# Performance work log

Measured on AMD Instinct MI355X. Metric: run time of the kernel, lower is better.

## Reference

```python
import jax, jax.numpy as jnp
import numpy as np

B, T, I, H = 32, 2048, 512, 512


def setup_inputs() -> dict:
    key = jax.random.key(0)
    ks = jax.random.split(key, 5)
    s_ih = 1.0 / np.sqrt(H)
    return {
        "x_t": jax.random.normal(ks[0], (B, T, I), dtype=jnp.float32),
        # PyTorch LSTM params, gate order [i, f, g, o]
        "W_ih": jax.random.uniform(ks[1], (4 * H, I), minval=-s_ih, maxval=s_ih, dtype=jnp.float32),
        "W_hh": jax.random.uniform(ks[2], (4 * H, H), minval=-s_ih, maxval=s_ih, dtype=jnp.float32),
        "b_ih": jax.random.uniform(ks[3], (4 * H,), minval=-s_ih, maxval=s_ih, dtype=jnp.float32),
        "b_hh": jax.random.uniform(ks[4], (4 * H,), minval=-s_ih, maxval=s_ih, dtype=jnp.float32),
    }


def _lstm_last_h(x_t, W_ih, W_hh, b_ih, b_hh):
    Bx = x_t.shape[0]
    Hh = W_hh.shape[1]
    # Precompute input projections for all timesteps in one big GEMM: [B,T,4H]
    x_proj = jnp.einsum("bti,gi->btg", x_t, W_ih) + (b_ih + b_hh)

    def step(carry, xp_t):
        h, c = carry
        z = xp_t + h @ W_hh.T  # [B, 4H]
        i, f, g, o = jnp.split(z, 4, axis=-1)
        i = jax.nn.sigmoid(i)
        f = jax.nn.sigmoid(f)
        g = jnp.tanh(g)
        o = jax.nn.sigmoid(o)
        c = f * c + i * g
        h = o * jnp.tanh(c)
        return (h, c), None

    h0 = jnp.zeros((Bx, Hh), dtype=x_t.dtype)
    c0 = jnp.zeros((Bx, Hh), dtype=x_t.dtype)
    (h_T, _), _ = jax.lax.scan(step, (h0, c0), jnp.swapaxes(x_proj, 0, 1))
    return h_T[None, :, :]  # [1, B, H] to match torch (num_layers*dirs, B, H)


def reference(x_t, W_ih, W_hh, b_ih, b_hh):
    return _lstm_last_h(x_t, W_ih, W_hh, b_ih, b_hh)
```

## Files before the change

kernel.cpp:

```cpp
#include <hip/hip_runtime.h>


#define T_FULL 2048
#define CHUNK  256
#define NCHUNK 8
#define NBLK   32

typedef float  f32x4 __attribute__((ext_vector_type(4)));
typedef short  s16x8 __attribute__((ext_vector_type(8)));

#define MFMA16(a,b,c) __builtin_amdgcn_mfma_f32_16x16x32_bf16((a),(b),(c),0,0,0)

__device__ inline unsigned short f2bf(float f){
  unsigned u = __builtin_bit_cast(unsigned, f);
  u += 0x7fffu + ((u>>16)&1u);
  return (unsigned short)(u>>16);
}
__device__ inline float bf2f(unsigned short s){
  unsigned u = ((unsigned)s)<<16;
  return __builtin_bit_cast(float, u);
}
__device__ inline float sigmoid_(float x){
  x = fminf(fmaxf(x,-30.f),30.f);
  return 1.f/(1.f + __expf(-x));
}
__device__ inline float tanh_(float x){
  x = fminf(fmaxf(x,-15.f),15.f);
  float e = __expf(2.f*x);
  return (e-1.f)/(e+1.f);
}

__global__ __launch_bounds__(256) void lstm_p1(
    const float* __restrict__ x, const float* __restrict__ Wih,
    const float* __restrict__ bih, const float* __restrict__ bhh,
    unsigned short* __restrict__ xp, int t0)
{
  __shared__ __align__(16) unsigned short At[64*136];
  __shared__ __align__(16) unsigned short Bt[64*136];
  const int tid = threadIdx.x, lane = tid&63, w = tid>>6;
  const int l15 = lane&15, l4 = lane>>4;
  const int n0 = blockIdx.x*64, m0 = blockIdx.y*64;
  const int mbase = (w&1)*32, nbase = (w>>1)*32;

  f32x4 acc[2][2];
  #pragma unroll
  for (int mi=0; mi<2; ++mi)
    #pragma unroll
    for (int ni=0; ni<2; ++ni)
      acc[mi][ni] = (f32x4){0.f,0.f,0.f,0.f};

  for (int kb=0; kb<4; ++kb){
    #pragma unroll
    for (int it=0; it<4; ++it){
      int grp = it*256 + tid;
      int row = grp>>4, c8 = (grp&15)*8;
      {
        int m = m0 + row;
        size_t t = (size_t)t0 + (m>>5), b = (size_t)(m&31);
        const float* src = x + ((b*2048 + t)<<9) + kb*128 + c8;
        f32x4 v0 = *(const f32x4*)src, v1 = *(const f32x4*)(src+4);
        unsigned short* d = &At[row*136 + c8];
        d[0]=f2bf(v0[0]); d[1]=f2bf(v0[1]); d[2]=f2bf(v0[2]); d[3]=f2bf(v0[3]);
        d[4]=f2bf(v1[0]); d[5]=f2bf(v1[1]); d[6]=f2bf(v1[2]); d[7]=f2bf(v1[3]);
      }
      {
        const float* src = Wih + (size_t)(n0+row)*512 + kb*128 + c8;
        f32x4 v0 = *(const f32x4*)src, v1 = *(const f32x4*)(src+4);
        unsigned short* d = &Bt[row*136 + c8];
        d[0]=f2bf(v0[0]); d[1]=f2bf(v0[1]); d[2]=f2bf(v0[2]); d[3]=f2bf(v0[3]);
        d[4]=f2bf(v1[0]); d[5]=f2bf(v1[1]); d[6]=f2bf(v1[2]); d[7]=f2bf(v1[3]);
      }
    }
    __syncthreads();
    #pragma unroll
    for (int ks=0; ks<4; ++ks){
      s16x8 af0 = *(const s16x8*)&At[(mbase+   l15)*136 + ks*32 + l4*8];
      s16x8 af1 = *(const s16x8*)&At[(mbase+16+l15)*136 + ks*32 + l4*8];
      s16x8 bf0 = *(const s16x8*)&Bt[(nbase+   l15)*136 + ks*32 + l4*8];
      s16x8 bf1 = *(const s16x8*)&Bt[(nbase+16+l15)*136 + ks*32 + l4*8];
      acc[0][0] = MFMA16(af0,bf0,acc[0][0]);
      acc[0][1] = MFMA16(af0,bf1,acc[0][1]);
      acc[1][0] = MFMA16(af1,bf0,acc[1][0]);
      acc[1][1] = MFMA16(af1,bf1,acc[1][1]);
    }
    __syncthreads();
  }
  #pragma unroll
  for (int ni=0; ni<2; ++ni){
    int col = n0 + nbase + ni*16 + l15;
    float bias = bih[col] + bhh[col];
    #pragma unroll
    for (int mi=0; mi<2; ++mi){
      #pragma unroll
      for (int r=0; r<4; ++r){
        int mrow = m0 + mbase + mi*16 + l4*4 + r;
        xp[(size_t)mrow*2048 + col] = f2bf(acc[mi][ni][r] + bias);
      }
    }
  }
}

__global__ __launch_bounds__(256) void lstm_p2(
    const unsigned short* __restrict__ xp, const float* __restrict__ Whh,
    unsigned short* __restrict__ Hbuf, float* __restrict__ cst,
    unsigned int* __restrict__ flag, float* __restrict__ out, int t0)
{
  const int k = blockIdx.x;
  const int tid = threadIdx.x;
  const int lane = tid & 63, w = tid >> 6;
  const int l15 = lane & 15, l4 = lane >> 4;
  const int mt = w & 1, gp = w >> 1;

  __shared__ __align__(16) char Hl[32*1024];
  __shared__ float zl[32][68];

  s16x8 wf[2][16];
  #pragma unroll
  for (int nt=0; nt<2; ++nt){
    int lrow = gp*32 + nt*16 + l15;
    int grow = (lrow>>4)*512 + k*16 + (lrow&15);
    const float* wr = Whh + (size_t)grow*512;
    #pragma unroll
    for (int ks=0; ks<16; ++ks){
      const float* s = wr + ks*32 + l4*8;
      f32x4 v0 = *(const f32x4*)s, v1 = *(const f32x4*)(s+4);
      s16x8 tt;
      tt[0]=(short)f2bf(v0[0]); tt[1]=(short)f2bf(v0[1]);
      tt[2]=(short)f2bf(v0[2]); tt[3]=(short)f2bf(v0[3]);
      tt[4]=(short)f2bf(v1[0]); tt[5]=(short)f2bf(v1[1]);
      tt[6]=(short)f2bf(v1[2]); tt[7]=(short)f2bf(v1[3]);
      wf[nt][ks] = tt;
    }
  }

  const int s_ = tid >> 3, a_ = tid & 7;
  const int ucol = k*16 + 2*a_;
  float c0 = cst[s_*512 + ucol], c1 = cst[s_*512 + ucol + 1];

  for (int tt=0; tt<CHUNK; ++tt){
    const int t = t0 + tt;

    unsigned int xq[4];
    #pragma unroll
    for (int g=0; g<4; ++g)
      xq[g] = *(const unsigned int*)(xp + (size_t)(tt*32 + s_)*2048 + g*512 + ucol);

    if (t > 0){
      if (w == 0){
        unsigned v;
        do {
          v = (lane < NBLK)
            ? __hip_atomic_load(&flag[lane<<5], __ATOMIC_RELAXED, __HIP_MEMORY_SCOPE_AGENT)
            : 0xffffffffu;
        } while (!__all(v >= (unsigned)t));
        __builtin_amdgcn_fence(__ATOMIC_ACQUIRE, "agent");
      }
      __syncthreads();
    }

    {
      const char* hsrc = (const char*)(Hbuf + ((t+1)&1)*(32*512));
      #pragma unroll
      for (int it=0; it<8; ++it){
        int off = (it*256 + tid)*16;
        f32x4 v = *(const f32x4*)(hsrc + off);
        *(f32x4*)&Hl[off ^ (((off>>10)&7)<<4)] = v;
      }
    }
    __syncthreads();

    f32x4 acc0 = (f32x4){0.f,0.f,0.f,0.f};
    f32x4 acc1 = (f32x4){0.f,0.f,0.f,0.f};
    {
      const int row = mt*16 + l15;
      const int swz = (row&7)<<4;
      const int rbase = row<<10;
      #pragma unroll
      for (int ks=0; ks<16; ++ks){
        int cb = ks*64 + l4*16;
        s16x8 af = *(const s16x8*)&Hl[rbase | (cb ^ swz)];
        acc0 = MFMA16(af, wf[0][ks], acc0);
        acc1 = MFMA16(af, wf[1][ks], acc1);
      }
    }
    #pragma unroll
    for (int r=0; r<4; ++r){
      zl[mt*16 + l4*4 + r][gp*32 +      l15] = acc0[r];
      zl[mt*16 + l4*4 + r][gp*32 + 16 + l15] = acc1[r];
    }
    __syncthreads();

    float zi0 = zl[s_][ 0 + 2*a_    ] + bf2f((unsigned short)(xq[0]&0xffffu));
    float zi1 = zl[s_][ 0 + 2*a_ + 1] + bf2f((unsigned short)(xq[0]>>16));
    float zf0 = zl[s_][16 + 2*a_    ] + bf2f((unsigned short)(xq[1]&0xffffu));
    float zf1 = zl[s_][16 + 2*a_ + 1] + bf2f((unsigned short)(xq[1]>>16));
    float zg0 = zl[s_][32 + 2*a_    ] + bf2f((unsigned short)(xq[2]&0xffffu));
    float zg1 = zl[s_][32 + 2*a_ + 1] + bf2f((unsigned short)(xq[2]>>16));
    float zo0 = zl[s_][48 + 2*a_    ] + bf2f((unsigned short)(xq[3]&0xffffu));
    float zo1 = zl[s_][48 + 2*a_ + 1] + bf2f((unsigned short)(xq[3]>>16));

    float i0 = sigmoid_(zi0), f0 = sigmoid_(zf0), g0 = tanh_(zg0), o0 = sigmoid_(zo0);
    float i1 = sigmoid_(zi1), f1 = sigmoid_(zf1), g1 = tanh_(zg1), o1 = sigmoid_(zo1);
    c0 = f0*c0 + i0*g0;
    c1 = f1*c1 + i1*g1;
    float h0 = o0 * tanh_(c0);
    float h1 = o1 * tanh_(c1);

    {
      unsigned short* hdst = Hbuf + (t&1)*(32*512);
      unsigned int hp = (unsigned int)f2bf(h0) | ((unsigned int)f2bf(h1)<<16);
      __hip_atomic_store((unsigned int*)((char*)hdst + s_*1024 + ucol*2), hp,
                         __ATOMIC_RELAXED, __HIP_MEMORY_SCOPE_AGENT);
    }
    if (t == T_FULL-1){
      out[s_*512 + ucol    ] = h0;
      out[s_*512 + ucol + 1] = h1;
    }

    asm volatile("s_waitcnt vmcnt(0)" ::: "memory");
    __syncthreads();
    if (tid == 0)
      __hip_atomic_store(&flag[k<<5], (unsigned)(t+1),
                         __ATOMIC_RELAXED, __HIP_MEMORY_SCOPE_AGENT);
  }

  cst[s_*512 + ucol    ] = c0;
  cst[s_*512 + ucol + 1] = c1;
}

extern "C" void kernel_launch(void* const* d_in, const int* in_sizes, int n_in,
                              void* d_out, int out_size, void* d_ws, size_t ws_size,
                              hipStream_t stream)
{
  const float* x   = (const float*)d_in[0];
  const float* Wih = (const float*)d_in[1];
  const float* Whh = (const float*)d_in[2];
  const float* bih = (const float*)d_in[3];
  const float* bhh = (const float*)d_in[4];
  float* out = (float*)d_out;

  char* ws = (char*)d_ws;
  const size_t XP_BYTES = (size_t)CHUNK*32*2048*2;
  unsigned short* xp   = (unsigned short*)ws;
  unsigned short* Hbuf = (unsigned short*)(ws + XP_BYTES);
  float*          cst  = (float*)(ws + XP_BYTES + 65536);
  unsigned int*   flag = (unsigned int*)(ws + XP_BYTES + 131072);

  (void)hipMemsetAsync(Hbuf, 0, 65536 + 65536 + 4096, stream);

  for (int c=0; c<NCHUNK; ++c){
    int t0 = c*CHUNK;
    lstm_p1<<<dim3(32, CHUNK*32/64), 256, 0, stream>>>(x, Wih, bih, bhh, xp, t0);
    lstm_p2<<<NBLK, 256, 0, stream>>>(xp, Whh, Hbuf, cst, flag, out, t0);
  }
}
```

Before: 6.382 ms.

## Replace per-step flag barrier with tagged hidden-state words polled directly

Each hidden-state element is now stored as a 32-bit word holding the bf16 value in its high half and the timestep tag in its low half, in a 4-deep ring buffer. Consumers poll the values directly from global memory until every tag matches, removing the separate flag array, the block-wide syncthreads and the staging of h in LDS. The gate layout is also remapped so that each wave owns whole units, with the four gates exchanged by lane shuffles rather than through shared memory. The cost is twice the global traffic for h, spinning on a full row load, and correctness that depends on the tagged words becoming visible atomically.

```diff
diff --git a/kernel.cpp b/kernel.cpp
--- a/kernel.cpp
+++ b/kernel.cpp
@@ -8,6 +8,8 @@
 
 typedef float  f32x4 __attribute__((ext_vector_type(4)));
 typedef short  s16x8 __attribute__((ext_vector_type(8)));
+typedef unsigned int u32;
+typedef u32    u32x4 __attribute__((ext_vector_type(4)));
 
 #define MFMA16(a,b,c) __builtin_amdgcn_mfma_f32_16x16x32_bf16((a),(b),(c),0,0,0)
 
@@ -100,26 +102,26 @@
   }
 }
 
-__global__ __launch_bounds__(256) void lstm_p2(
+__global__ __launch_bounds__(256,1) void lstm_p2(
     const unsigned short* __restrict__ xp, const float* __restrict__ Whh,
-    unsigned short* __restrict__ Hbuf, float* __restrict__ cst,
-    unsigned int* __restrict__ flag, float* __restrict__ out, int t0)
+    u32* __restrict__ H32, float* __restrict__ cst,
+    float* __restrict__ out, int t0)
 {
   const int k = blockIdx.x;
   const int tid = threadIdx.x;
   const int lane = tid & 63, w = tid >> 6;
   const int l15 = lane & 15, l4 = lane >> 4;
-  const int mt = w & 1, gp = w >> 1;
-
-  __shared__ __align__(16) char Hl[32*1024];
-  __shared__ float zl[32][68];
-
-  s16x8 wf[2][16];
-  #pragma unroll
-  for (int nt=0; nt<2; ++nt){
-    int lrow = gp*32 + nt*16 + l15;
-    int grow = (lrow>>4)*512 + k*16 + (lrow&15);
-    const float* wr = Whh + (size_t)grow*512;
+  const int u_local = l15 >> 2, g = l15 & 3;
+  const int U = k*16 + w*4 + u_local;
+  const int gcol = g*512 + U;
+
+  const int q = g;
+  const int mt_q = q >> 1, rr = (q & 1) * 2;
+  const int bq = mt_q*16 + l4*4 + rr;
+
+  s16x8 wf[16];
+  {
+    const float* wr = Whh + (size_t)(g*512 + U)*512;
     #pragma unroll
     for (int ks=0; ks<16; ++ks){
       const float* s = wr + ks*32 + l4*8;
@@ -129,103 +131,117 @@
       tt[2]=(short)f2bf(v0[2]); tt[3]=(short)f2bf(v0[3]);
       tt[4]=(short)f2bf(v1[0]); tt[5]=(short)f2bf(v1[1]);
       tt[6]=(short)f2bf(v1[2]); tt[7]=(short)f2bf(v1[3]);
-      wf[nt][ks] = tt;
-    }
-  }
-
-  const int s_ = tid >> 3, a_ = tid & 7;
-  const int ucol = k*16 + 2*a_;
-  float c0 = cst[s_*512 + ucol], c1 = cst[s_*512 + ucol + 1];
+      wf[ks] = tt;
+    }
+  }
+
+  float c[2][4];
+  #pragma unroll
+  for (int mt2=0; mt2<2; ++mt2)
+    #pragma unroll
+    for (int r=0; r<4; ++r)
+      c[mt2][r] = cst[(size_t)(mt2*16 + l4*4 + r)*512 + U];
 
   for (int tt=0; tt<CHUNK; ++tt){
     const int t = t0 + tt;
-
-    unsigned int xq[4];
-    #pragma unroll
-    for (int g=0; g<4; ++g)
-      xq[g] = *(const unsigned int*)(xp + (size_t)(tt*32 + s_)*2048 + g*512 + ucol);
-
-    if (t > 0){
-      if (w == 0){
-        unsigned v;
-        do {
-          v = (lane < NBLK)
-            ? __hip_atomic_load(&flag[lane<<5], __ATOMIC_RELAXED, __HIP_MEMORY_SCOPE_AGENT)
-            : 0xffffffffu;
-        } while (!__all(v >= (unsigned)t));
+    const u32 tagc = (u32)t, tagn = (u32)(t+1);
+    const u32* Hs = H32 + (size_t)(t & 3)*16384;
+    u32*       Hd = H32 + (size_t)((t+1) & 3)*16384;
+
+    float xg[2][4];
+    #pragma unroll
+    for (int mt2=0; mt2<2; ++mt2)
+      #pragma unroll
+      for (int r=0; r<4; ++r)
+        xg[mt2][r] = bf2f(xp[(size_t)(tt*32 + mt2*16 + l4*4 + r)*2048 + gcol]);
+
+    f32x4 z[2];
+    #pragma unroll
+    for (int mt2=0; mt2<2; ++mt2){
+      u32x4 A0[16], A1[16];
+      u32 bad;
+      do {
         __builtin_amdgcn_fence(__ATOMIC_ACQUIRE, "agent");
-      }
-      __syncthreads();
+        const u32* rowp = Hs + (mt2*16 + l15)*512 + l4*8;
+        #pragma unroll
+        for (int ks=0; ks<16; ++ks){
+          A0[ks] = *(const u32x4*)(rowp + ks*32);
+          A1[ks] = *(const u32x4*)(rowp + ks*32 + 4);
+        }
+        bad = 0;
+        #pragma unroll
+        for (int ks=0; ks<16; ++ks){
+          #pragma unroll
+          for (int j=0; j<4; ++j){
+            bad |= (A0[ks][j] ^ tagc);
+            bad |= (A1[ks][j] ^ tagc);
+          }
+        }
+        bad &= 0xffffu;
+      } while (__any(bad != 0));
+
+      f32x4 acc = (f32x4){0.f,0.f,0.f,0.f};
+      #pragma unroll
+      for (int ks=0; ks<16; ++ks){
+        u32x4 p;
+        p[0] = (A0[ks][0] >> 16) | (A0[ks][1] & 0xffff0000u);
+        p[1] = (A0[ks][2] >> 16) | (A0[ks][3] & 0xffff0000u);
+        p[2] = (A1[ks][0] >> 16) | (A1[ks][1] & 0xffff0000u);
+        p[3] = (A1[ks][2] >> 16) | (A1[ks][3] & 0xffff0000u);
+        s16x8 af = __builtin_bit_cast(s16x8, p);
+        acc = MFMA16(af, wf[ks], acc);
+      }
+      z[mt2] = acc;
+    }
+
+    float hv[2][4];
+    #pragma unroll
+    for (int mt2=0; mt2<2; ++mt2){
+      #pragma unroll
+      for (int r=0; r<4; ++r){
+        float v = z[mt2][r] + xg[mt2][r];
+        float vi = __shfl_xor(v, g    );
+        float vf = __shfl_xor(v, g ^ 1);
+        float vg = __shfl_xor(v, g ^ 2);
+        float vo = __shfl_xor(v, g ^ 3);
+        float ii = sigmoid_(vi), ff = sigmoid_(vf);
+        float gg = tanh_(vg),    oo = sigmoid_(vo);
+        float cc = ff*c[mt2][r] + ii*gg;
+        c[mt2][r] = cc;
+        hv[mt2][r] = oo * tanh_(cc);
+      }
     }
 
     {
-      const char* hsrc = (const char*)(Hbuf + ((t+1)&1)*(32*512));
-      #pragma unroll
-      for (int it=0; it<8; ++it){
-        int off = (it*256 + tid)*16;
-        f32x4 v = *(const f32x4*)(hsrc + off);
-        *(f32x4*)&Hl[off ^ (((off>>10)&7)<<4)] = v;
-      }
-    }
-    __syncthreads();
-
-    f32x4 acc0 = (f32x4){0.f,0.f,0.f,0.f};
-    f32x4 acc1 = (f32x4){0.f,0.f,0.f,0.f};
-    {
-      const int row = mt*16 + l15;
-      const int swz = (row&7)<<4;
-      const int rbase = row<<10;
-      #pragma unroll
-      for (int ks=0; ks<16; ++ks){
-        int cb = ks*64 + l4*16;
-        s16x8 af = *(const s16x8*)&Hl[rbase | (cb ^ swz)];
-        acc0 = MFMA16(af, wf[0][ks], acc0);
-        acc1 = MFMA16(af, wf[1][ks], acc1);
-      }
-    }
-    #pragma unroll
-    for (int r=0; r<4; ++r){
-      zl[mt*16 + l4*4 + r][gp*32 +      l15] = acc0[r];
-      zl[mt*16 + l4*4 + r][gp*32 + 16 + l15] = acc1[r];
-    }
-    __syncthreads();
-
-    float zi0 = zl[s_][ 0 + 2*a_    ] + bf2f((unsigned short)(xq[0]&0xffffu));
-    float zi1 = zl[s_][ 0 + 2*a_ + 1] + bf2f((unsigned short)(xq[0]>>16));
-    float zf0 = zl[s_][16 + 2*a_    ] + bf2f((unsigned short)(xq[1]&0xffffu));
-    float zf1 = zl[s_][16 + 2*a_ + 1] + bf2f((unsigned short)(xq[1]>>16));
-    float zg0 = zl[s_][32 + 2*a_    ] + bf2f((unsigned short)(xq[2]&0xffffu));
-    float zg1 = zl[s_][32 + 2*a_ + 1] + bf2f((unsigned short)(xq[2]>>16));
-    float zo0 = zl[s_][48 + 2*a_    ] + bf2f((unsigned short)(xq[3]&0xffffu));
-    float zo1 = zl[s_][48 + 2*a_ + 1] + bf2f((unsigned short)(xq[3]>>16));
-
-    float i0 = sigmoid_(zi0), f0 = sigmoid_(zf0), g0 = tanh_(zg0), o0 = sigmoid_(zo0);
-    float i1 = sigmoid_(zi1), f1 = sigmoid_(zf1), g1 = tanh_(zg1), o1 = sigmoid_(zo1);
-    c0 = f0*c0 + i0*g0;
-    c1 = f1*c1 + i1*g1;
-    float h0 = o0 * tanh_(c0);
-    float h1 = o1 * tanh_(c1);
-
-    {
-      unsigned short* hdst = Hbuf + (t&1)*(32*512);
-      unsigned int hp = (unsigned int)f2bf(h0) | ((unsigned int)f2bf(h1)<<16);
-      __hip_atomic_store((unsigned int*)((char*)hdst + s_*1024 + ucol*2), hp,
+      float ha0 = (q&1) ? hv[0][2] : hv[0][0];
+      float ha1 = (q&1) ? hv[0][3] : hv[0][1];
+      float hb0 = (q&1) ? hv[1][2] : hv[1][0];
+      float hb1 = (q&1) ? hv[1][3] : hv[1][1];
+      float h0 = (q>>1) ? hb0 : ha0;
+      float h1 = (q>>1) ? hb1 : ha1;
+      u32 w0 = ((u32)f2bf(h0) << 16) | tagn;
+      u32 w1 = ((u32)f2bf(h1) << 16) | tagn;
+      __hip_atomic_store(&Hd[(size_t)(bq  )*512 + U], w0,
                          __ATOMIC_RELAXED, __HIP_MEMORY_SCOPE_AGENT);
-    }
-    if (t == T_FULL-1){
-      out[s_*512 + ucol    ] = h0;
-      out[s_*512 + ucol + 1] = h1;
-    }
-
-    asm volatile("s_waitcnt vmcnt(0)" ::: "memory");
-    __syncthreads();
-    if (tid == 0)
-      __hip_atomic_store(&flag[k<<5], (unsigned)(t+1),
+      __hip_atomic_store(&Hd[(size_t)(bq+1)*512 + U], w1,
                          __ATOMIC_RELAXED, __HIP_MEMORY_SCOPE_AGENT);
-  }
-
-  cst[s_*512 + ucol    ] = c0;
-  cst[s_*512 + ucol + 1] = c1;
+      if (t == T_FULL-1){
+        out[(size_t)(bq  )*512 + U] = h0;
+        out[(size_t)(bq+1)*512 + U] = h1;
+      }
+    }
+  }
+
+  {
+    float ca0 = (q&1) ? c[0][2] : c[0][0];
+    float ca1 = (q&1) ? c[0][3] : c[0][1];
+    float cb0 = (q&1) ? c[1][2] : c[1][0];
+    float cb1 = (q&1) ? c[1][3] : c[1][1];
+    float c0s = (q>>1) ? cb0 : ca0;
+    float c1s = (q>>1) ? cb1 : ca1;
+    cst[(size_t)(bq  )*512 + U] = c0s;
+    cst[(size_t)(bq+1)*512 + U] = c1s;
+  }
 }
 
 extern "C" void kernel_launch(void* const* d_in, const int* in_sizes, int n_in,
@@ -241,16 +257,15 @@
 
   char* ws = (char*)d_ws;
   const size_t XP_BYTES = (size_t)CHUNK*32*2048*2;
-  unsigned short* xp   = (unsigned short*)ws;
-  unsigned short* Hbuf = (unsigned short*)(ws + XP_BYTES);
-  float*          cst  = (float*)(ws + XP_BYTES + 65536);
-  unsigned int*   flag = (unsigned int*)(ws + XP_BYTES + 131072);
-
-  (void)hipMemsetAsync(Hbuf, 0, 65536 + 65536 + 4096, stream);
+  unsigned short* xp  = (unsigned short*)ws;
+  u32*            H32 = (u32*)(ws + XP_BYTES);
+  float*          cst = (float*)(ws + XP_BYTES + 262144);
+
+  (void)hipMemsetAsync(H32, 0, 262144 + 65536, stream);
 
   for (int c=0; c<NCHUNK; ++c){
     int t0 = c*CHUNK;
     lstm_p1<<<dim3(32, CHUNK*32/64), 256, 0, stream>>>(x, Wih, bih, bhh, xp, t0);
-    lstm_p2<<<NBLK, 256, 0, stream>>>(xp, Whh, Hbuf, cst, flag, out, t0);
-  }
-}
+    lstm_p2<<<NBLK, 256, 0, stream>>>(xp, Whh, H32, cst, out, t0);
+  }
+}
```

After: 24.98 ms. 3.91x slower.

## Split recurrent step into 128 single-wave blocks with per-batch-half sync groups

Applied to the files above, without the earlier changes.

The recurrent kernel changes from 32 four-wave blocks to 128 single-wave blocks, split into two independent batch halves of 64 blocks that each sync only among themselves through a 4-deep H ring buffer. Each wave loads its h fragments directly from global memory into registers instead of staging through LDS. Gate nonlinearities are combined via lane shuffles, which removes the LDS z-exchange and all __syncthreads from the step. The aim is to cut per-step latency on the serial critical path. In exchange it adds more spinning blocks polling flags and more global h reads per block.

```diff
diff --git a/kernel.cpp b/kernel.cpp
--- a/kernel.cpp
+++ b/kernel.cpp
@@ -4,10 +4,10 @@
 #define T_FULL 2048
 #define CHUNK  256
 #define NCHUNK 8
-#define NBLK   32
 
 typedef float  f32x4 __attribute__((ext_vector_type(4)));
 typedef short  s16x8 __attribute__((ext_vector_type(8)));
+typedef unsigned int u32;
 
 #define MFMA16(a,b,c) __builtin_amdgcn_mfma_f32_16x16x32_bf16((a),(b),(c),0,0,0)
 
@@ -100,132 +100,135 @@
   }
 }
 
-__global__ __launch_bounds__(256) void lstm_p2(
+__global__ __launch_bounds__(64,1) void lstm_p2(
     const unsigned short* __restrict__ xp, const float* __restrict__ Whh,
     unsigned short* __restrict__ Hbuf, float* __restrict__ cst,
-    unsigned int* __restrict__ flag, float* __restrict__ out, int t0)
+    u32* __restrict__ flag, float* __restrict__ out, int t0)
 {
-  const int k = blockIdx.x;
-  const int tid = threadIdx.x;
-  const int lane = tid & 63, w = tid >> 6;
+  const int lane = threadIdx.x;
+  const int c = blockIdx.x >> 6, s = blockIdx.x & 63;
   const int l15 = lane & 15, l4 = lane >> 4;
-  const int mt = w & 1, gp = w >> 1;
-
-  __shared__ __align__(16) char Hl[32*1024];
-  __shared__ float zl[32][68];
-
-  s16x8 wf[2][16];
+  const int g = l15 & 3, uq = l15 >> 2;
+  const int u0 = s*8 + uq, u1 = u0 + 4;
+
+  s16x8 wf0[16], wf1[16];
+  {
+    const float* w0 = Whh + (size_t)(g*512 + u0)*512 + l4*8;
+    const float* w1 = Whh + (size_t)(g*512 + u1)*512 + l4*8;
+    #pragma unroll
+    for (int ks=0; ks<16; ++ks){
+      f32x4 a0 = *(const f32x4*)(w0 + ks*32), b0 = *(const f32x4*)(w0 + ks*32 + 4);
+      f32x4 a1 = *(const f32x4*)(w1 + ks*32), b1 = *(const f32x4*)(w1 + ks*32 + 4);
+      s16x8 t0v, t1v;
+      t0v[0]=(short)f2bf(a0[0]); t0v[1]=(short)f2bf(a0[1]);
+      t0v[2]=(short)f2bf(a0[2]); t0v[3]=(short)f2bf(a0[3]);
+      t0v[4]=(short)f2bf(b0[0]); t0v[5]=(short)f2bf(b0[1]);
+      t0v[6]=(short)f2bf(b0[2]); t0v[7]=(short)f2bf(b0[3]);
+      t1v[0]=(short)f2bf(a1[0]); t1v[1]=(short)f2bf(a1[1]);
+      t1v[2]=(short)f2bf(a1[2]); t1v[3]=(short)f2bf(a1[3]);
+      t1v[4]=(short)f2bf(b1[0]); t1v[5]=(short)f2bf(b1[1]);
+      t1v[6]=(short)f2bf(b1[2]); t1v[7]=(short)f2bf(b1[3]);
+      wf0[ks] = t0v; wf1[ks] = t1v;
+    }
+  }
+
+  float c0[4], c1[4];
   #pragma unroll
-  for (int nt=0; nt<2; ++nt){
-    int lrow = gp*32 + nt*16 + l15;
-    int grow = (lrow>>4)*512 + k*16 + (lrow&15);
-    const float* wr = Whh + (size_t)grow*512;
-    #pragma unroll
-    for (int ks=0; ks<16; ++ks){
-      const float* s = wr + ks*32 + l4*8;
-      f32x4 v0 = *(const f32x4*)s, v1 = *(const f32x4*)(s+4);
-      s16x8 tt;
-      tt[0]=(short)f2bf(v0[0]); tt[1]=(short)f2bf(v0[1]);
-      tt[2]=(short)f2bf(v0[2]); tt[3]=(short)f2bf(v0[3]);
-      tt[4]=(short)f2bf(v1[0]); tt[5]=(short)f2bf(v1[1]);
-      tt[6]=(short)f2bf(v1[2]); tt[7]=(short)f2bf(v1[3]);
-      wf[nt][ks] = tt;
-    }
-  }
-
-  const int s_ = tid >> 3, a_ = tid & 7;
-  const int ucol = k*16 + 2*a_;
-  float c0 = cst[s_*512 + ucol], c1 = cst[s_*512 + ucol + 1];
+  for (int r=0; r<4; ++r){
+    c0[r] = cst[(size_t)(c*16 + l4*4 + r)*512 + u0];
+    c1[r] = cst[(size_t)(c*16 + l4*4 + r)*512 + u1];
+  }
 
   for (int tt=0; tt<CHUNK; ++tt){
     const int t = t0 + tt;
 
-    unsigned int xq[4];
-    #pragma unroll
-    for (int g=0; g<4; ++g)
-      xq[g] = *(const unsigned int*)(xp + (size_t)(tt*32 + s_)*2048 + g*512 + ucol);
-
-    if (t > 0){
-      if (w == 0){
-        unsigned v;
-        do {
-          v = (lane < NBLK)
-            ? __hip_atomic_load(&flag[lane<<5], __ATOMIC_RELAXED, __HIP_MEMORY_SCOPE_AGENT)
-            : 0xffffffffu;
-        } while (!__all(v >= (unsigned)t));
-        __builtin_amdgcn_fence(__ATOMIC_ACQUIRE, "agent");
-      }
-      __syncthreads();
-    }
-
-    {
-      const char* hsrc = (const char*)(Hbuf + ((t+1)&1)*(32*512));
+    float xg0[4], xg1[4];
+    {
+      const unsigned short* xrow = xp + (size_t)(tt*32 + c*16)*2048 + g*512;
       #pragma unroll
-      for (int it=0; it<8; ++it){
-        int off = (it*256 + tid)*16;
-        f32x4 v = *(const f32x4*)(hsrc + off);
-        *(f32x4*)&Hl[off ^ (((off>>10)&7)<<4)] = v;
-      }
-    }
-    __syncthreads();
+      for (int r=0; r<4; ++r){
+        xg0[r] = bf2f(xrow[(size_t)(l4*4+r)*2048 + u0]);
+        xg1[r] = bf2f(xrow[(size_t)(l4*4+r)*2048 + u1]);
+      }
+    }
+
+    {
+      u32 v;
+      do {
+        v = (lane == s) ? (u32)t
+          : __hip_atomic_load(&flag[(u32)((c<<6) | lane) << 4],
+                              __ATOMIC_RELAXED, __HIP_MEMORY_SCOPE_AGENT);
+      } while (__any(v < (u32)t));
+    }
+    __builtin_amdgcn_fence(__ATOMIC_ACQUIRE, "agent");
+
+    s16x8 hf[16];
+    {
+      const unsigned short* Hs = Hbuf + (size_t)((c<<2) | (t&3))*8192 + l15*512 + l4*8;
+      #pragma unroll
+      for (int ks=0; ks<16; ++ks)
+        hf[ks] = *(const s16x8*)(Hs + ks*32);
+    }
 
     f32x4 acc0 = (f32x4){0.f,0.f,0.f,0.f};
     f32x4 acc1 = (f32x4){0.f,0.f,0.f,0.f};
-    {
-      const int row = mt*16 + l15;
-      const int swz = (row&7)<<4;
-      const int rbase = row<<10;
-      #pragma unroll
-      for (int ks=0; ks<16; ++ks){
-        int cb = ks*64 + l4*16;
-        s16x8 af = *(const s16x8*)&Hl[rbase | (cb ^ swz)];
-        acc0 = MFMA16(af, wf[0][ks], acc0);
-        acc1 = MFMA16(af, wf[1][ks], acc1);
-      }
-    }
+    #pragma unroll
+    for (int ks=0; ks<16; ++ks){
+      acc0 = MFMA16(hf[ks], wf0[ks], acc0);
+      acc1 = MFMA16(hf[ks], wf1[ks], acc1);
+    }
+
+    float hv0[4], hv1[4];
     #pragma unroll
     for (int r=0; r<4; ++r){
-      zl[mt*16 + l4*4 + r][gp*32 +      l15] = acc0[r];
-      zl[mt*16 + l4*4 + r][gp*32 + 16 + l15] = acc1[r];
-    }
-    __syncthreads();
-
-    float zi0 = zl[s_][ 0 + 2*a_    ] + bf2f((unsigned short)(xq[0]&0xffffu));
-    float zi1 = zl[s_][ 0 + 2*a_ + 1] + bf2f((unsigned short)(xq[0]>>16));
-    float zf0 = zl[s_][16 + 2*a_    ] + bf2f((unsigned short)(xq[1]&0xffffu));
-    float zf1 = zl[s_][16 + 2*a_ + 1] + bf2f((unsigned short)(xq[1]>>16));
-    float zg0 = zl[s_][32 + 2*a_    ] + bf2f((unsigned short)(xq[2]&0xffffu));
-    float zg1 = zl[s_][32 + 2*a_ + 1] + bf2f((unsigned short)(xq[2]>>16));
-    float zo0 = zl[s_][48 + 2*a_    ] + bf2f((unsigned short)(xq[3]&0xffffu));
-    float zo1 = zl[s_][48 + 2*a_ + 1] + bf2f((unsigned short)(xq[3]>>16));
-
-    float i0 = sigmoid_(zi0), f0 = sigmoid_(zf0), g0 = tanh_(zg0), o0 = sigmoid_(zo0);
-    float i1 = sigmoid_(zi1), f1 = sigmoid_(zf1), g1 = tanh_(zg1), o1 = sigmoid_(zo1);
-    c0 = f0*c0 + i0*g0;
-    c1 = f1*c1 + i1*g1;
-    float h0 = o0 * tanh_(c0);
-    float h1 = o1 * tanh_(c1);
-
-    {
-      unsigned short* hdst = Hbuf + (t&1)*(32*512);
-      unsigned int hp = (unsigned int)f2bf(h0) | ((unsigned int)f2bf(h1)<<16);
-      __hip_atomic_store((unsigned int*)((char*)hdst + s_*1024 + ucol*2), hp,
+      float v = acc0[r] + xg0[r];
+      float vi = __shfl_xor(v, g    );
+      float vf = __shfl_xor(v, g ^ 1);
+      float vg = __shfl_xor(v, g ^ 2);
+      float vo = __shfl_xor(v, g ^ 3);
+      float ii = sigmoid_(vi), ff = sigmoid_(vf), gg = tanh_(vg), oo = sigmoid_(vo);
+      float cc = ff*c0[r] + ii*gg; c0[r] = cc; hv0[r] = oo*tanh_(cc);
+      v = acc1[r] + xg1[r];
+      vi = __shfl_xor(v, g    );
+      vf = __shfl_xor(v, g ^ 1);
+      vg = __shfl_xor(v, g ^ 2);
+      vo = __shfl_xor(v, g ^ 3);
+      ii = sigmoid_(vi); ff = sigmoid_(vf); gg = tanh_(vg); oo = sigmoid_(vo);
+      cc = ff*c1[r] + ii*gg; c1[r] = cc; hv1[r] = oo*tanh_(cc);
+    }
+
+    float hsel0 = (g&1) ? ((g&2) ? hv0[3] : hv0[1]) : ((g&2) ? hv0[2] : hv0[0]);
+    float hsel1 = (g&1) ? ((g&2) ? hv1[3] : hv1[1]) : ((g&2) ? hv1[2] : hv1[0]);
+
+    {
+      unsigned short* Hd = Hbuf + (size_t)((c<<2) | ((t+1)&3))*8192;
+      u32 hb0 = f2bf(hsel0), hb1 = f2bf(hsel1);
+      u32 o0 = (u32)__shfl_xor((int)hb0, 4);
+      u32 o1 = (u32)__shfl_xor((int)hb1, 4);
+      if ((uq & 1) == 0){
+        __hip_atomic_store((u32*)(Hd + (l4*4+g)*512 + u0), hb0 | (o0<<16),
+                           __ATOMIC_RELAXED, __HIP_MEMORY_SCOPE_AGENT);
+        __hip_atomic_store((u32*)(Hd + (l4*4+g)*512 + u1), hb1 | (o1<<16),
+                           __ATOMIC_RELAXED, __HIP_MEMORY_SCOPE_AGENT);
+      }
+      if (t == T_FULL-1){
+        out[(size_t)(c*16 + l4*4 + g)*512 + u0] = hsel0;
+        out[(size_t)(c*16 + l4*4 + g)*512 + u1] = hsel1;
+      }
+    }
+
+    asm volatile("s_waitcnt vmcnt(0)" ::: "memory");
+    if (lane == 0)
+      __hip_atomic_store(&flag[(u32)((c<<6) | s) << 4], (u32)(t+1),
                          __ATOMIC_RELAXED, __HIP_MEMORY_SCOPE_AGENT);
-    }
-    if (t == T_FULL-1){
-      out[s_*512 + ucol    ] = h0;
-      out[s_*512 + ucol + 1] = h1;
-    }
-
-    asm volatile("s_waitcnt vmcnt(0)" ::: "memory");
-    __syncthreads();
-    if (tid == 0)
-      __hip_atomic_store(&flag[k<<5], (unsigned)(t+1),
-                         __ATOMIC_RELAXED, __HIP_MEMORY_SCOPE_AGENT);
-  }
-
-  cst[s_*512 + ucol    ] = c0;
-  cst[s_*512 + ucol + 1] = c1;
+  }
+
+  {
+    float cs0 = (g&1) ? ((g&2) ? c0[3] : c0[1]) : ((g&2) ? c0[2] : c0[0]);
+    float cs1 = (g&1) ? ((g&2) ? c1[3] : c1[1]) : ((g&2) ? c1[2] : c1[0]);
+    cst[(size_t)(c*16 + l4*4 + g)*512 + u0] = cs0;
+    cst[(size_t)(c*16 + l4*4 + g)*512 + u1] = cs1;
+  }
 }
 
 extern "C" void kernel_launch(void* const* d_in, const int* in_sizes, int n_in,
@@ -243,14 +246,14 @@
   const size_t XP_BYTES = (size_t)CHUNK*32*2048*2;
   unsigned short* xp   = (unsigned short*)ws;
   unsigned short* Hbuf = (unsigned short*)(ws + XP_BYTES);
-  float*          cst  = (float*)(ws + XP_BYTES + 65536);
-  unsigned int*   flag = (unsigned int*)(ws + XP_BYTES + 131072);
-
-  (void)hipMemsetAsync(Hbuf, 0, 65536 + 65536 + 4096, stream);
+  float*          cst  = (float*)(ws + XP_BYTES + 131072);
+  u32*            flag = (u32*)(ws + XP_BYTES + 131072 + 65536);
+
+  (void)hipMemsetAsync(Hbuf, 0, 131072 + 65536 + 8192, stream);
 
   for (int c=0; c<NCHUNK; ++c){
     int t0 = c*CHUNK;
     lstm_p1<<<dim3(32, CHUNK*32/64), 256, 0, stream>>>(x, Wih, bih, bhh, xp, t0);
-    lstm_p2<<<NBLK, 256, 0, stream>>>(xp, Whh, Hbuf, cst, flag, out, t0);
-  }
-}
+    lstm_p2<<<128, 64, 0, stream>>>(xp, Whh, Hbuf, cst, flag, out, t0);
+  }
+}
```

After: 12.94 ms. 2.03x slower.

## Overlap next-chunk input projection GEMM with recurrent LSTM steps in one fused launch

Applied to the files above, without the earlier changes.

Fuses the input-projection GEMM and the recurrent kernel into one launch. Blocks 0–31 run the recurrence on the current chunk, while the other 224 blocks compute the next chunk's projection into a double buffer. The chunk size is halved so more chunks can pipeline, and the flag spin loop is unrolled to keep two loads in flight. The recurrence blocks must share CUs with the GEMM blocks, which adds bandwidth contention and could slow the latency-bound serial steps.

```diff
diff --git a/kernel.cpp b/kernel.cpp
--- a/kernel.cpp
+++ b/kernel.cpp
@@ -2,12 +2,14 @@
 
 
 #define T_FULL 2048
-#define CHUNK  256
-#define NCHUNK 8
+#define CHUNK  128
+#define NCHUNK 16
 #define NBLK   32
+#define NGEMM  224
 
 typedef float  f32x4 __attribute__((ext_vector_type(4)));
 typedef short  s16x8 __attribute__((ext_vector_type(8)));
+typedef unsigned int u32;
 
 #define MFMA16(a,b,c) __builtin_amdgcn_mfma_f32_16x16x32_bf16((a),(b),(c),0,0,0)
 
@@ -30,16 +32,16 @@
   return (e-1.f)/(e+1.f);
 }
 
-__global__ __launch_bounds__(256) void lstm_p1(
-    const float* __restrict__ x, const float* __restrict__ Wih,
-    const float* __restrict__ bih, const float* __restrict__ bhh,
-    unsigned short* __restrict__ xp, int t0)
-{
-  __shared__ __align__(16) unsigned short At[64*136];
-  __shared__ __align__(16) unsigned short Bt[64*136];
+__device__ void gemm_tile(const float* __restrict__ x, const float* __restrict__ Wih,
+                          const float* __restrict__ bih, const float* __restrict__ bhh,
+                          unsigned short* __restrict__ xp, int t0, int nx, int ny,
+                          char* smem)
+{
+  unsigned short* At = (unsigned short*)smem;
+  unsigned short* Bt = (unsigned short*)(smem + 17408);
   const int tid = threadIdx.x, lane = tid&63, w = tid>>6;
   const int l15 = lane&15, l4 = lane>>4;
-  const int n0 = blockIdx.x*64, m0 = blockIdx.y*64;
+  const int n0 = nx*64, m0 = ny*64;
   const int mbase = (w&1)*32, nbase = (w>>1)*32;
 
   f32x4 acc[2][2];
@@ -100,19 +102,42 @@
   }
 }
 
-__global__ __launch_bounds__(256) void lstm_p2(
-    const unsigned short* __restrict__ xp, const float* __restrict__ Whh,
+__global__ __launch_bounds__(256) void lstm_p1(
+    const float* __restrict__ x, const float* __restrict__ Wih,
+    const float* __restrict__ bih, const float* __restrict__ bhh,
+    unsigned short* __restrict__ xp, int t0)
+{
+  __shared__ __align__(16) char smem[34816];
+  gemm_tile(x, Wih, bih, bhh, xp, t0, blockIdx.x, blockIdx.y, smem);
+}
+
+__global__ __launch_bounds__(256,1) void lstm_fused(
+    const unsigned short* __restrict__ xp_cur,
+    const float* __restrict__ x, const float* __restrict__ Wih,
+    const float* __restrict__ bih, const float* __restrict__ bhh,
+    unsigned short* __restrict__ xp_next, const float* __restrict__ Whh,
     unsigned short* __restrict__ Hbuf, float* __restrict__ cst,
-    unsigned int* __restrict__ flag, float* __restrict__ out, int t0)
-{
-  const int k = blockIdx.x;
+    u32* __restrict__ flag, float* __restrict__ out, int t0, int do_gemm)
+{
+  __shared__ __align__(16) char smem[41472];
+  const int bid = blockIdx.x;
+
+  if (bid >= NBLK){
+    if (do_gemm){
+      const int t0n = t0 + CHUNK;
+      for (int tile = bid - NBLK; tile < 32*(CHUNK*32/64); tile += NGEMM)
+        gemm_tile(x, Wih, bih, bhh, xp_next, t0n, tile & 31, tile >> 5, smem);
+    }
+    return;
+  }
+
+  char* Hl = smem;
+  float (*zl)[68] = (float(*)[68])(smem + 32768);
+  const int k = bid;
   const int tid = threadIdx.x;
   const int lane = tid & 63, w = tid >> 6;
   const int l15 = lane & 15, l4 = lane >> 4;
   const int mt = w & 1, gp = w >> 1;
-
-  __shared__ __align__(16) char Hl[32*1024];
-  __shared__ float zl[32][68];
 
   s16x8 wf[2][16];
   #pragma unroll
@@ -124,12 +149,12 @@
     for (int ks=0; ks<16; ++ks){
       const float* s = wr + ks*32 + l4*8;
       f32x4 v0 = *(const f32x4*)s, v1 = *(const f32x4*)(s+4);
-      s16x8 tt;
-      tt[0]=(short)f2bf(v0[0]); tt[1]=(short)f2bf(v0[1]);
-      tt[2]=(short)f2bf(v0[2]); tt[3]=(short)f2bf(v0[3]);
-      tt[4]=(short)f2bf(v1[0]); tt[5]=(short)f2bf(v1[1]);
-      tt[6]=(short)f2bf(v1[2]); tt[7]=(short)f2bf(v1[3]);
-      wf[nt][ks] = tt;
+      s16x8 tv;
+      tv[0]=(short)f2bf(v0[0]); tv[1]=(short)f2bf(v0[1]);
+      tv[2]=(short)f2bf(v0[2]); tv[3]=(short)f2bf(v0[3]);
+      tv[4]=(short)f2bf(v1[0]); tv[5]=(short)f2bf(v1[1]);
+      tv[6]=(short)f2bf(v1[2]); tv[7]=(short)f2bf(v1[3]);
+      wf[nt][ks] = tv;
     }
   }
 
@@ -143,16 +168,23 @@
     unsigned int xq[4];
     #pragma unroll
     for (int g=0; g<4; ++g)
-      xq[g] = *(const unsigned int*)(xp + (size_t)(tt*32 + s_)*2048 + g*512 + ucol);
+      xq[g] = *(const unsigned int*)(xp_cur + (size_t)(tt*32 + s_)*2048 + g*512 + ucol);
 
     if (t > 0){
       if (w == 0){
-        unsigned v;
-        do {
-          v = (lane < NBLK)
+        u32 va = (lane < NBLK)
+          ? __hip_atomic_load(&flag[lane<<5], __ATOMIC_RELAXED, __HIP_MEMORY_SCOPE_AGENT)
+          : 0xffffffffu;
+        for (;;){
+          u32 vb = (lane < NBLK)
             ? __hip_atomic_load(&flag[lane<<5], __ATOMIC_RELAXED, __HIP_MEMORY_SCOPE_AGENT)
             : 0xffffffffu;
-        } while (!__all(v >= (unsigned)t));
+          if (__all(va >= (u32)t)) break;
+          va = (lane < NBLK)
+            ? __hip_atomic_load(&flag[lane<<5], __ATOMIC_RELAXED, __HIP_MEMORY_SCOPE_AGENT)
+            : 0xffffffffu;
+          if (__all(vb >= (u32)t)) break;
+        }
         __builtin_amdgcn_fence(__ATOMIC_ACQUIRE, "agent");
       }
       __syncthreads();
@@ -240,17 +272,22 @@
   float* out = (float*)d_out;
 
   char* ws = (char*)d_ws;
-  const size_t XP_BYTES = (size_t)CHUNK*32*2048*2;
-  unsigned short* xp   = (unsigned short*)ws;
-  unsigned short* Hbuf = (unsigned short*)(ws + XP_BYTES);
-  float*          cst  = (float*)(ws + XP_BYTES + 65536);
-  unsigned int*   flag = (unsigned int*)(ws + XP_BYTES + 131072);
+  const size_t XPB = (size_t)CHUNK*32*2048*2;
+  unsigned short* xp0  = (unsigned short*)ws;
+  unsigned short* xp1  = (unsigned short*)(ws + XPB);
+  unsigned short* Hbuf = (unsigned short*)(ws + 2*XPB);
+  float*          cst  = (float*)(ws + 2*XPB + 65536);
+  u32*            flag = (u32*)(ws + 2*XPB + 65536 + 65536);
 
   (void)hipMemsetAsync(Hbuf, 0, 65536 + 65536 + 4096, stream);
 
+  lstm_p1<<<dim3(32, CHUNK*32/64), 256, 0, stream>>>(x, Wih, bih, bhh, xp0, 0);
+
   for (int c=0; c<NCHUNK; ++c){
-    int t0 = c*CHUNK;
-    lstm_p1<<<dim3(32, CHUNK*32/64), 256, 0, stream>>>(x, Wih, bih, bhh, xp, t0);
-    lstm_p2<<<NBLK, 256, 0, stream>>>(xp, Whh, Hbuf, cst, flag, out, t0);
-  }
-}
+    unsigned short* xc = (c & 1) ? xp1 : xp0;
+    unsigned short* xn = (c & 1) ? xp0 : xp1;
+    lstm_fused<<<256, 256, 0, stream>>>(xc, x, Wih, bih, bhh, xn, Whh,
+                                        Hbuf, cst, flag, out, c*CHUNK,
+                                        (c < NCHUNK-1) ? 1 : 0);
+  }
+}
```

Measured after the change: 6.088 ms (median of 2 runs). 1.05x faster.
